# Optimization experiments

Hardware: AMD Instinct MI355X
Metric: run time of the kernel (lower is better)

The kernel has to match this reference:

```python
import jax, jax.numpy as jnp
import numpy as np

STRIDE = (1, 1)
PAD = 1


def setup_inputs() -> dict:
    key = jax.random.key(0)
    k1, k2, k3 = jax.random.split(key, 3)
    X = jax.random.normal(k1, (32, 128, 56, 56), dtype=jnp.float32)
    weight = jax.random.normal(k2, (256, 128, 3, 3), dtype=jnp.float32) * 0.05
    bias = jax.random.normal(k3, (256,), dtype=jnp.float32) * 0.05
    return {"X": X, "weight": weight, "bias": bias}


def reference(X, weight, bias):
    # Equivalent to the naive 8-loop conv: standard 2D cross-correlation,
    # NCHW input, OIHW weight, stride 1, padding 1.
    out = jax.lax.conv_general_dilated(
        X, weight,
        window_strides=STRIDE,
        padding=[(PAD, PAD), (PAD, PAD)],
        dimension_numbers=("NCHW", "OIHW", "NCHW"),
    )
    out = out + bias[None, :, None, None]
    return out
```

## Files before the change

### kernel.cpp

```cpp
#include <hip/hip_runtime.h>
#include <hip/hip_bf16.h>


typedef __attribute__((ext_vector_type(8))) _Float16 half8;
typedef __attribute__((ext_vector_type(4))) float floatx4;

#define NN    32
#define CC    128
#define HH    56
#define WW    56
#define KOUT  256
#define HWs   3136
#define HP    58
#define HPP   (HP * HP)
#define XP_SHORTS ((size_t)NN * HPP * CC)
#define WT_SHORTS (36 * 8192)
#define WS_NEED ((XP_SHORTS + WT_SHORTS) * sizeof(short))

__device__ __forceinline__ void gload_lds16(const void* g, void* l) {
    __builtin_amdgcn_global_load_lds(
        (const __attribute__((address_space(1))) unsigned int*)g,
        (__attribute__((address_space(3))) unsigned int*)l, 16, 0, 0);
}

__global__ __launch_bounds__(256) void prep_x(const float* __restrict__ X,
                                              short* __restrict__ Xp) {
    __shared__ float xl[128 * 57];
    const int n = blockIdx.x / HH;
    const int h = blockIdx.x % HH;
    const float* src = X + (size_t)n * CC * HWs + h * WW;
    const int tid = threadIdx.x;
#pragma unroll
    for (int it = 0; it < 28; ++it) {
        const int idx = it * 256 + tid;
        const int c = idx / 56;
        const int w = idx - c * 56;
        xl[c * 57 + w] = src[(size_t)c * HWs + w];
    }
    __syncthreads();
#pragma unroll
    for (int it = 0; it < 4; ++it) {
        const int u = it * 256 + tid;
        if (u < 896) {
            const int oct = u & 15, w = u >> 4;
            _Float16 v[8];
#pragma unroll
            for (int j = 0; j < 8; ++j)
                v[j] = (_Float16)xl[(oct * 8 + j) * 57 + w];
            *(half8*)&Xp[((size_t)n * HPP + (h + 1) * HP + (w + 1)) * CC + oct * 8] =
                *(half8*)v;
        }
    }
}

__global__ __launch_bounds__(256) void prep_w3(const float* __restrict__ Wsrc,
                                               short* __restrict__ Wt) {
    const int gid = blockIdx.x * 256 + threadIdx.x;
    const int t2  = gid >> 10;
    const int u8  = gid & 1023;
    const int r   = u8 >> 3;
    const int o   = u8 & 7;
    const int rs  = t2 >> 2;
    const int ct  = (t2 >> 1) & 1;
    const int kb  = t2 & 1;
    const int k   = kb * 128 + r;
    const int c0  = ct * 64 + ((o ^ (r & 7)) << 3);
    _Float16 v[8];
#pragma unroll
    for (int j = 0; j < 8; ++j)
        v[j] = (_Float16)Wsrc[((size_t)k * CC + c0 + j) * 9 + rs];
    *(half8*)&Wt[(size_t)t2 * 8192 + u8 * 8] = *(half8*)v;
}

__global__ __launch_bounds__(256, 2) void conv_mfma3(
    const short* __restrict__ Xp, const short* __restrict__ Wt,
    const float* __restrict__ bias, float* __restrict__ out) {

    __shared__ __align__(16) short smem[32768];

    const int tid  = threadIdx.x;
    const int lane = tid & 63;
    const int wid  = tid >> 6;
    const int wr   = wid >> 1;
    const int wc   = wid & 1;
    const int bid  = blockIdx.x;
    const int kblk = blockIdx.y;
    const int pblk = (bid & 7) * 98 + (bid >> 3);

    const int swzoct = (lane & 7) ^ (lane >> 3);
    const short* vsrc[4];
#pragma unroll
    for (int i = 0; i < 4; ++i) {
        const int row = wid * 32 + i * 8 + (lane >> 3);
        const int p   = pblk * 128 + row;
        const int n   = p / HWs;
        const int hw  = p % HWs;
        const int h   = hw / WW;
        const int w   = hw % WW;
        vsrc[i] = Xp + ((size_t)n * HPP + (h + 1) * HP + (w + 1)) * CC + swzoct * 8;
    }

#define STAGE(kk, bb) do {                                                     \
    const int rs_ = (kk) >> 1, ct_ = (kk) & 1;                                 \
    const int tap_ = ((rs_ / 3 - 1) * HP + (rs_ % 3 - 1)) * CC + ct_ * 64;     \
    const short* as_ = Wt + (size_t)((kk) * 2 + kblk) * 8192 + wid * 2048      \
                       + lane * 8;                                             \
    _Pragma("unroll")                                                          \
    for (int i_ = 0; i_ < 4; ++i_)                                             \
        gload_lds16(as_ + i_ * 512, &smem[(bb) + wid * 2048 + i_ * 512]);      \
    _Pragma("unroll")                                                          \
    for (int i_ = 0; i_ < 4; ++i_)                                             \
        gload_lds16(vsrc[i_] + tap_, &smem[(bb) + 8192 + wid * 2048 + i_ * 512]); \
} while (0)

    floatx4 acc[4][4];
#pragma unroll
    for (int i = 0; i < 4; i++)
#pragma unroll
        for (int j = 0; j < 4; j++) acc[i][j] = (floatx4)(0.0f);

    STAGE(0, 0);
    __syncthreads();

    int cur = 0;
    for (int k = 0; k < 18; ++k) {
        const int cb = cur * 16384;
        if (k < 17) STAGE(k + 1, 16384 - cb);

#pragma unroll
        for (int ksub = 0; ksub < 2; ++ksub) {
            const int koct = ksub * 4 + (lane >> 4);
            half8 ah[4], bh[4];
#pragma unroll
            for (int mt = 0; mt < 4; ++mt) {
                const int ar = wr * 64 + mt * 16 + (lane & 15);
                ah[mt] = *(const half8*)&smem[cb + ar * 64 + ((koct ^ (ar & 7)) << 3)];
            }
#pragma unroll
            for (int nt = 0; nt < 4; ++nt) {
                const int br = wc * 64 + nt * 16 + (lane & 15);
                bh[nt] = *(const half8*)&smem[cb + 8192 + br * 64 + ((koct ^ (br & 7)) << 3)];
            }
#pragma unroll
            for (int mt = 0; mt < 4; ++mt)
#pragma unroll
                for (int nt = 0; nt < 4; ++nt)
                    acc[mt][nt] = __builtin_amdgcn_mfma_f32_16x16x32_f16(
                        ah[mt], bh[nt], acc[mt][nt], 0, 0, 0);
        }

        __syncthreads();
        cur ^= 1;
    }
#undef STAGE

#pragma unroll
    for (int mt = 0; mt < 4; ++mt) {
        const int ch = kblk * 128 + wr * 64 + mt * 16 + ((lane >> 4) << 2);
#pragma unroll
        for (int nt = 0; nt < 4; ++nt) {
            const int p  = pblk * 128 + wc * 64 + nt * 16 + (lane & 15);
            const int n  = p / HWs;
            const int hw = p % HWs;
            float* ob = out + ((size_t)n * KOUT + ch) * HWs + hw;
#pragma unroll
            for (int r = 0; r < 4; ++r)
                ob[(size_t)r * HWs] = acc[mt][nt][r] + bias[ch + r];
        }
    }
}

__global__ __launch_bounds__(256) void conv_naive(const float* __restrict__ X,
                                                  const float* __restrict__ Wt,
                                                  const float* __restrict__ bias,
                                                  float* __restrict__ out) {
    long o = (long)blockIdx.x * 256 + threadIdx.x;
    int w_ = o % WW;
    long t1 = o / WW;
    int h_ = t1 % HH;
    long t2 = t1 / HH;
    int k_ = t2 % KOUT;
    int n_ = (int)(t2 / KOUT);
    float acc = bias[k_];
    for (int c = 0; c < CC; ++c)
        for (int r = 0; r < 3; ++r) {
            int ih = h_ + r - 1;
            if ((unsigned)ih >= 56u) continue;
            for (int s = 0; s < 3; ++s) {
                int iw = w_ + s - 1;
                if ((unsigned)iw >= 56u) continue;
                acc += X[((long)(n_ * CC + c) * HH + ih) * WW + iw] *
                       Wt[((k_ * CC + c) * 3 + r) * 3 + s];
            }
        }
    out[o] = acc;
}

extern "C" void kernel_launch(void* const* d_in, const int* in_sizes, int n_in,
                              void* d_out, int out_size, void* d_ws, size_t ws_size,
                              hipStream_t stream) {
    const float* X    = (const float*)d_in[0];
    const float* Wsrc = (const float*)d_in[1];
    const float* bias = (const float*)d_in[2];
    float* out        = (float*)d_out;

    if (ws_size >= WS_NEED) {
        short* Xp = (short*)d_ws;
        short* Wt = Xp + XP_SHORTS;
        hipMemsetAsync(Xp, 0, XP_SHORTS * sizeof(short), stream);
        prep_x<<<NN * HH, 256, 0, stream>>>(X, Xp);
        prep_w3<<<144, 256, 0, stream>>>(Wsrc, Wt);
        conv_mfma3<<<dim3(784, 2), 256, 0, stream>>>(Xp, Wt, bias, out);
    } else {
        conv_naive<<<100352, 256, 0, stream>>>(X, Wsrc, bias, out);
    }
}
```

Baseline: 215.0 us.

## Fuse padding into prep kernel, single-buffer conv LDS for higher occupancy

The separate memset of the padded input buffer is removed; the prep kernel now also writes the zero border rows and columns and loads the input with 4-wide vector reads. The conv kernel drops double buffering, halving LDS to 32 KB per block and raising the launch-bounds occupancy target from 2 to 3 blocks per CU. Without double buffering, global-to-LDS loads no longer overlap the MFMA work within a block and an extra barrier runs each iteration. The design relies on the extra resident blocks to hide that latency instead.

```diff
diff --git a/kernel.cpp b/kernel.cpp
--- a/kernel.cpp
+++ b/kernel.cpp
@@ -23,19 +23,36 @@
         (__attribute__((address_space(3))) unsigned int*)l, 16, 0, 0);
 }
 
-__global__ __launch_bounds__(256) void prep_x(const float* __restrict__ X,
-                                              short* __restrict__ Xp) {
+__global__ __launch_bounds__(256) void prep_x2(const float* __restrict__ X,
+                                               short* __restrict__ Xp) {
+    const int n   = blockIdx.x / HP;
+    const int hp  = blockIdx.x % HP;
+    const int tid = threadIdx.x;
+    short* dst = Xp + ((size_t)n * HPP + (size_t)hp * HP) * CC;
+
+    half8 z = {(_Float16)0.f, (_Float16)0.f, (_Float16)0.f, (_Float16)0.f,
+               (_Float16)0.f, (_Float16)0.f, (_Float16)0.f, (_Float16)0.f};
+
+    if (hp == 0 || hp == HP - 1) {
+#pragma unroll
+        for (int it = 0; it < 4; ++it) {
+            const int u = it * 256 + tid;
+            if (u < 928) *(half8*)&dst[u * 8] = z;
+        }
+        return;
+    }
+
+    const int h = hp - 1;
     __shared__ float xl[128 * 57];
-    const int n = blockIdx.x / HH;
-    const int h = blockIdx.x % HH;
     const float* src = X + (size_t)n * CC * HWs + h * WW;
-    const int tid = threadIdx.x;
-#pragma unroll
-    for (int it = 0; it < 28; ++it) {
-        const int idx = it * 256 + tid;
-        const int c = idx / 56;
-        const int w = idx - c * 56;
-        xl[c * 57 + w] = src[(size_t)c * HWs + w];
+#pragma unroll
+    for (int i = 0; i < 7; ++i) {
+        const int idx = i * 256 + tid;
+        const int c   = idx / 14;
+        const int w4  = idx - c * 14;
+        const floatx4 v = *(const floatx4*)&src[(size_t)c * HWs + w4 * 4];
+#pragma unroll
+        for (int k = 0; k < 4; ++k) xl[c * 57 + w4 * 4 + k] = v[k];
     }
     __syncthreads();
 #pragma unroll
@@ -47,8 +64,12 @@
 #pragma unroll
             for (int j = 0; j < 8; ++j)
                 v[j] = (_Float16)xl[(oct * 8 + j) * 57 + w];
-            *(half8*)&Xp[((size_t)n * HPP + (h + 1) * HP + (w + 1)) * CC + oct * 8] =
-                *(half8*)v;
+            *(half8*)&dst[(w + 1) * CC + oct * 8] = *(half8*)v;
+        } else if (u < 928) {
+            const int q = u - 896;
+            const int oct = q & 15;
+            const int wpad = (q >> 4) ? (HP - 1) : 0;
+            *(half8*)&dst[wpad * CC + oct * 8] = z;
         }
     }
 }
@@ -72,11 +93,11 @@
     *(half8*)&Wt[(size_t)t2 * 8192 + u8 * 8] = *(half8*)v;
 }
 
-__global__ __launch_bounds__(256, 2) void conv_mfma3(
+__global__ __launch_bounds__(256, 3) void conv_mfma4(
     const short* __restrict__ Xp, const short* __restrict__ Wt,
     const float* __restrict__ bias, float* __restrict__ out) {
 
-    __shared__ __align__(16) short smem[32768];
+    __shared__ __align__(16) short smem[16384];
 
     const int tid  = threadIdx.x;
     const int lane = tid & 63;
@@ -100,32 +121,27 @@
         vsrc[i] = Xp + ((size_t)n * HPP + (h + 1) * HP + (w + 1)) * CC + swzoct * 8;
     }
 
-#define STAGE(kk, bb) do {                                                     \
-    const int rs_ = (kk) >> 1, ct_ = (kk) & 1;                                 \
-    const int tap_ = ((rs_ / 3 - 1) * HP + (rs_ % 3 - 1)) * CC + ct_ * 64;     \
-    const short* as_ = Wt + (size_t)((kk) * 2 + kblk) * 8192 + wid * 2048      \
-                       + lane * 8;                                             \
-    _Pragma("unroll")                                                          \
-    for (int i_ = 0; i_ < 4; ++i_)                                             \
-        gload_lds16(as_ + i_ * 512, &smem[(bb) + wid * 2048 + i_ * 512]);      \
-    _Pragma("unroll")                                                          \
-    for (int i_ = 0; i_ < 4; ++i_)                                             \
-        gload_lds16(vsrc[i_] + tap_, &smem[(bb) + 8192 + wid * 2048 + i_ * 512]); \
-} while (0)
-
     floatx4 acc[4][4];
 #pragma unroll
     for (int i = 0; i < 4; i++)
 #pragma unroll
         for (int j = 0; j < 4; j++) acc[i][j] = (floatx4)(0.0f);
 
-    STAGE(0, 0);
-    __syncthreads();
-
-    int cur = 0;
     for (int k = 0; k < 18; ++k) {
-        const int cb = cur * 16384;
-        if (k < 17) STAGE(k + 1, 16384 - cb);
+        const int rs = k >> 1, ct = k & 1;
+        const int tap = ((rs / 3 - 1) * HP + (rs % 3 - 1)) * CC + ct * 64;
+
+        if (k) __syncthreads();
+
+        const short* as_ = Wt + (size_t)(k * 2 + kblk) * 8192 + wid * 2048 + lane * 8;
+#pragma unroll
+        for (int i = 0; i < 4; ++i)
+            gload_lds16(as_ + i * 512, &smem[wid * 2048 + i * 512]);
+#pragma unroll
+        for (int i = 0; i < 4; ++i)
+            gload_lds16(vsrc[i] + tap, &smem[8192 + wid * 2048 + i * 512]);
+
+        __syncthreads();
 
 #pragma unroll
         for (int ksub = 0; ksub < 2; ++ksub) {
@@ -134,12 +150,12 @@
 #pragma unroll
             for (int mt = 0; mt < 4; ++mt) {
                 const int ar = wr * 64 + mt * 16 + (lane & 15);
-                ah[mt] = *(const half8*)&smem[cb + ar * 64 + ((koct ^ (ar & 7)) << 3)];
+                ah[mt] = *(const half8*)&smem[ar * 64 + ((koct ^ (ar & 7)) << 3)];
             }
 #pragma unroll
             for (int nt = 0; nt < 4; ++nt) {
                 const int br = wc * 64 + nt * 16 + (lane & 15);
-                bh[nt] = *(const half8*)&smem[cb + 8192 + br * 64 + ((koct ^ (br & 7)) << 3)];
+                bh[nt] = *(const half8*)&smem[8192 + br * 64 + ((koct ^ (br & 7)) << 3)];
             }
 #pragma unroll
             for (int mt = 0; mt < 4; ++mt)
@@ -148,11 +164,7 @@
                     acc[mt][nt] = __builtin_amdgcn_mfma_f32_16x16x32_f16(
                         ah[mt], bh[nt], acc[mt][nt], 0, 0, 0);
         }
-
-        __syncthreads();
-        cur ^= 1;
-    }
-#undef STAGE
+    }
 
 #pragma unroll
     for (int mt = 0; mt < 4; ++mt) {
@@ -207,10 +219,9 @@
     if (ws_size >= WS_NEED) {
         short* Xp = (short*)d_ws;
         short* Wt = Xp + XP_SHORTS;
-        hipMemsetAsync(Xp, 0, XP_SHORTS * sizeof(short), stream);
-        prep_x<<<NN * HH, 256, 0, stream>>>(X, Xp);
+        prep_x2<<<NN * HP, 256, 0, stream>>>(X, Xp);
         prep_w3<<<144, 256, 0, stream>>>(Wsrc, Wt);
-        conv_mfma3<<<dim3(784, 2), 256, 0, stream>>>(Xp, Wt, bias, out);
+        conv_mfma4<<<dim3(784, 2), 256, 0, stream>>>(Xp, Wt, bias, out);
     } else {
         conv_naive<<<100352, 256, 0, stream>>>(X, Wsrc, bias, out);
     }
```

Measured after the change: 213.3 us. Within noise of the previous version (-0.8%).
